# Optimization experiments

Hardware: AMD Instinct MI355X
Metric: run time of the kernel (lower is better)

The kernel has to match this reference:

```python
import jax, jax.numpy as jnp
import numpy as np

B, N, DIM, H, K = 2, 8192, 256, 8, 32
HD = DIM // H


def setup_inputs() -> dict:
    key = jax.random.key(0)
    ks = jax.random.split(key, 10)
    s = 1.0 / np.sqrt(DIM)
    return {
        "x": jax.random.normal(ks[0], (B, N, DIM), jnp.float32),
        "xyz": jax.random.normal(ks[1], (B, N, 3), jnp.float32),
        "idx": jax.random.randint(ks[2], (B, N, K), 0, N, jnp.int32),
        "Wq": jax.random.normal(ks[3], (DIM, DIM), jnp.float32) * s,
        "bq": jnp.zeros((DIM,), jnp.float32),
        "Wk": jax.random.normal(ks[4], (DIM, DIM), jnp.float32) * s,
        "bk": jnp.zeros((DIM,), jnp.float32),
        "Wv": jax.random.normal(ks[5], (DIM, DIM), jnp.float32) * s,
        "bv": jnp.zeros((DIM,), jnp.float32),
        "Wo": jax.random.normal(ks[6], (DIM, DIM), jnp.float32) * s,
        "bo": jnp.zeros((DIM,), jnp.float32),
        "W1": jax.random.normal(ks[7], (3, 32), jnp.float32) * 0.5,
        "b1": jnp.zeros((32,), jnp.float32),
        "W2": jax.random.normal(ks[8], (32, H), jnp.float32) * 0.2,
        "b2": jnp.zeros((H,), jnp.float32),
    }


def reference(x, xyz, idx, Wq, bq, Wk, bk, Wv, bv, Wo, bo, W1, b1, W2, b2):
    Bn, Nn, C = x.shape
    k = idx.shape[-1]
    q = (x @ Wq + bq).reshape(Bn, Nn, H, HD)          # [B,N,H,hd]
    kf = (x @ Wk + bk).reshape(Bn, Nn, H, HD)
    vf = (x @ Wv + bv).reshape(Bn, Nn, H, HD)
    # gather k neighbors per point (per-batch fancy indexing)
    gather = jax.vmap(lambda f, i: f[i])               # [N,H,hd],[N,k] -> [N,k,H,hd]
    kn = gather(kf, idx)                               # [B,N,k,H,hd]
    vn = gather(vf, idx)
    nxyz = jax.vmap(lambda p, i: p[i])(xyz, idx)       # [B,N,k,3]
    rel = xyz[:, :, None, :] - nxyz                    # [B,N,k,3]
    bias = jax.nn.relu(rel @ W1 + b1) @ W2 + b2        # [B,N,k,H]
    scores = jnp.einsum('bnhd,bnkhd->bnhk', q, kn) / np.sqrt(HD).astype(np.float32)
    scores = scores + bias.transpose(0, 1, 3, 2)       # [B,N,H,k]
    attn = jax.nn.softmax(scores, axis=-1)
    out = jnp.einsum('bnhk,bnkhd->bnhd', attn, vn).reshape(Bn, Nn, C)
    return out @ Wo + bo
```

## Files before the change

kernel.cpp:

```cpp
#include <hip/hip_runtime.h>
#include <hip/hip_bf16.h>

typedef unsigned int uint32;
typedef unsigned short ushort;
typedef __attribute__((ext_vector_type(4))) float floatx4;
typedef __attribute__((ext_vector_type(8))) __bf16 bf16x8;

#define NPTS 8192
#define HSZ 524288

__device__ __forceinline__ ushort f2bf(float f) {
    uint32 u = __float_as_uint(f);
    uint32 r = (u + 0x7fffu + ((u >> 16) & 1u)) >> 16;
    return (ushort)r;
}
__device__ __forceinline__ float bf1(ushort u) { return __uint_as_float((uint32)u << 16); }
__device__ __forceinline__ float bflo(uint32 u) { return __uint_as_float(u << 16); }
__device__ __forceinline__ float bfhi(uint32 u) { return __uint_as_float(u & 0xffff0000u); }

__global__ __launch_bounds__(256) void prep_kernel(
    const float* __restrict__ x, const float* __restrict__ xyz, const int* __restrict__ idx,
    const float* __restrict__ Wq, const float* __restrict__ Wk,
    const float* __restrict__ Wv, const float* __restrict__ Wo,
    const float* __restrict__ bq, const float* __restrict__ bk, const float* __restrict__ bv,
    const float* __restrict__ W1, const float* __restrict__ b1,
    const float* __restrict__ W2, const float* __restrict__ b2,
    ushort* __restrict__ xb, ushort* __restrict__ Wqkvt, ushort* __restrict__ Wot,
    float* __restrict__ biasqkv, ushort* __restrict__ bias_hg, uint32* __restrict__ offs) {
    const int bi = blockIdx.x;
    const int tid = threadIdx.x;
    if (bi < 4096) {
        int i = (bi * 256 + tid) * 4;
        float4 v = *(const float4*)(x + i);
        ushort4 o;
        o.x = f2bf(v.x); o.y = f2bf(v.y); o.z = f2bf(v.z); o.w = f2bf(v.w);
        *(ushort4*)(xb + i) = o;
    } else if (bi < 5120) {
        int f = (bi - 4096) * 256 + tid;
        if (f < 768 * 256) {
            int n = f >> 8, k = f & 255;
            int seg = n >> 8, nc = n & 255;
            const float* W = (seg == 0) ? Wq : (seg == 1) ? Wk : Wv;
            Wqkvt[f] = f2bf(W[k * 256 + nc]);
        } else {
            int g = f - 768 * 256;
            int n = g >> 8, k = g & 255;
            Wot[g] = f2bf(Wo[k * 256 + n]);
        }
        if (f < 768) biasqkv[f] = (f < 256) ? bq[f] : (f < 512) ? bk[f - 256] : bv[f - 512];
    } else {
        __shared__ float W1s[96], b1s[32], W2s[256], b2s[8];
        if (tid < 96) W1s[tid] = W1[tid];
        if (tid < 32) b1s[tid] = b1[tid];
        W2s[tid] = W2[tid];
        if (tid < 8) b2s[tid] = b2[tid];
        __syncthreads();
        const int wid = tid >> 6, lane = tid & 63;
        const int s = lane >> 5, j = lane & 31;
        const int p = (bi - 5120) * 8 + wid * 2 + s;
        const int b = p >> 13, n = p & 8191;
        const int nj = idx[(size_t)p * 32 + j];
        offs[(size_t)p * 32 + j] = (uint32)(nj + b * NPTS) * 64u;
        const size_t pb = ((size_t)b * NPTS + n) * 3;
        const size_t nb = ((size_t)b * NPTS + nj) * 3;
        const float rx = xyz[pb + 0] - xyz[nb + 0];
        const float ry = xyz[pb + 1] - xyz[nb + 1];
        const float rz = xyz[pb + 2] - xyz[nb + 2];
        float acc[8];
#pragma unroll
        for (int h = 0; h < 8; ++h) acc[h] = b2s[h];
#pragma unroll
        for (int u = 0; u < 32; ++u) {
            float hv = rx * W1s[u] + ry * W1s[32 + u] + rz * W1s[64 + u] + b1s[u];
            hv = fmaxf(hv, 0.f);
#pragma unroll
            for (int h = 0; h < 8; ++h) acc[h] += hv * W2s[u * 8 + h];
        }
#pragma unroll
        for (int h = 0; h < 8; ++h) bias_hg[(size_t)h * HSZ + p * 32 + j] = f2bf(acc[h]);
    }
}

__global__ __launch_bounds__(256) void gemm_qkv(const ushort* __restrict__ A,
                                                const ushort* __restrict__ Wt,
                                                const float* __restrict__ bias,
                                                ushort* __restrict__ qh, ushort* __restrict__ kh,
                                                ushort* __restrict__ vh) {
    __shared__ __align__(16) ushort As[128 * 64];
    __shared__ __align__(16) ushort Bs[128 * 64];
    const int tid = threadIdx.x;
    const int w = tid >> 6, lane = tid & 63;
    const int m0 = blockIdx.y * 128, n0 = blockIdx.x * 128;
    const int wm = (w & 1) * 64, wn = (w >> 1) * 64;

    floatx4 acc[4][4] = {};

    for (int kt = 0; kt < 256; kt += 64) {
        __syncthreads();
#pragma unroll
        for (int c4 = 0; c4 < 4; ++c4) {
            const int c = w * 4 + c4;
            const int r = c * 8 + (lane >> 3);
            const int gseg = (lane & 7) ^ (r & 7);
            const char* ga = (const char*)(A + (size_t)(m0 + r) * 256 + kt) + gseg * 16;
            const char* gb = (const char*)(Wt + (size_t)(n0 + r) * 256 + kt) + gseg * 16;
            __builtin_amdgcn_global_load_lds((const __attribute__((address_space(1))) void*)ga,
                                             (__attribute__((address_space(3))) void*)((char*)As + c * 1024),
                                             16, 0, 0);
            __builtin_amdgcn_global_load_lds((const __attribute__((address_space(1))) void*)gb,
                                             (__attribute__((address_space(3))) void*)((char*)Bs + c * 1024),
                                             16, 0, 0);
        }
        __syncthreads();

        bf16x8 af[2][4], bg[2][4];
#pragma unroll
        for (int kk = 0; kk < 2; ++kk) {
            const int s = kk * 4 + (lane >> 4);
            const int phys = s ^ (lane & 7);
#pragma unroll
            for (int i = 0; i < 4; ++i) {
                af[kk][i] = *(const bf16x8*)((const char*)As + (wm + i * 16 + (lane & 15)) * 128 + phys * 16);
                bg[kk][i] = *(const bf16x8*)((const char*)Bs + (wn + i * 16 + (lane & 15)) * 128 + phys * 16);
            }
        }
#pragma unroll
        for (int kk = 0; kk < 2; ++kk)
#pragma unroll
            for (int fi = 0; fi < 4; ++fi)
#pragma unroll
                for (int pi = 0; pi < 4; ++pi)
                    acc[fi][pi] = __builtin_amdgcn_mfma_f32_16x16x32_bf16(bg[kk][fi], af[kk][pi], acc[fi][pi], 0, 0, 0);
    }

#pragma unroll
    for (int fi = 0; fi < 4; ++fi) {
        const int gf0 = n0 + wn + fi * 16 + (lane >> 4) * 4;
        const int seg = gf0 >> 8;
        const int head = (gf0 >> 5) & 7;
        const int dim0 = gf0 & 31;
        ushort* segp = (seg == 0) ? qh : (seg == 1) ? kh : vh;
        const float b0 = bias[gf0 + 0], b1v = bias[gf0 + 1];
        const float b2v = bias[gf0 + 2], b3v = bias[gf0 + 3];
#pragma unroll
        for (int pi = 0; pi < 4; ++pi) {
            const int pt = m0 + wm + pi * 16 + (lane & 15);
            uint2 o;
            o.x = (uint32)f2bf(acc[fi][pi][0] + b0) | ((uint32)f2bf(acc[fi][pi][1] + b1v) << 16);
            o.y = (uint32)f2bf(acc[fi][pi][2] + b2v) | ((uint32)f2bf(acc[fi][pi][3] + b3v) << 16);
            *(uint2*)(segp + (size_t)head * HSZ + (size_t)pt * 32 + dim0) = o;
        }
    }
}

__global__ __launch_bounds__(256) void gemm_mfma64(const ushort* __restrict__ A,
                                                   const ushort* __restrict__ Wt,
                                                   const float* __restrict__ bias,
                                                   float* __restrict__ outv, int N) {
    __shared__ __align__(16) ushort As[64 * 32];
    __shared__ __align__(16) ushort Bs[64 * 32];
    const int tid = threadIdx.x;
    const int w = tid >> 6, lane = tid & 63;
    const int m0 = blockIdx.y * 64, n0 = blockIdx.x * 64;
    const int row = tid >> 2;
    const int col16 = (tid & 3) * 16;

    floatx4 acc[4] = {};

    for (int kt = 0; kt < 256; kt += 32) {
        __syncthreads();
        {
            const char* ga = (const char*)(A + (size_t)(m0 + row) * 256 + kt) + col16;
            const char* gb = (const char*)(Wt + (size_t)(n0 + row) * 256 + kt) + col16;
            __builtin_amdgcn_global_load_lds((const __attribute__((address_space(1))) void*)ga,
                                             (__attribute__((address_space(3))) void*)((char*)As + w * 1024),
                                             16, 0, 0);
            __builtin_amdgcn_global_load_lds((const __attribute__((address_space(1))) void*)gb,
                                             (__attribute__((address_space(3))) void*)((char*)Bs + w * 1024),
                                             16, 0, 0);
        }
        __syncthreads();

        bf16x8 af = *(const bf16x8*)&As[(w * 16 + (lane & 15)) * 32 + (lane >> 4) * 8];
        bf16x8 bg[4];
#pragma unroll
        for (int ni = 0; ni < 4; ++ni)
            bg[ni] = *(const bf16x8*)&Bs[(ni * 16 + (lane & 15)) * 32 + (lane >> 4) * 8];
#pragma unroll
        for (int ni = 0; ni < 4; ++ni)
            acc[ni] = __builtin_amdgcn_mfma_f32_16x16x32_bf16(af, bg[ni], acc[ni], 0, 0, 0);
    }

#pragma unroll
    for (int ni = 0; ni < 4; ++ni) {
        const int col = n0 + ni * 16 + (lane & 15);
        const float bv = bias[col];
        const int row0 = m0 + w * 16 + (lane >> 4) * 4;
#pragma unroll
        for (int r = 0; r < 4; ++r)
            outv[(size_t)(row0 + r) * N + col] = acc[ni][r] + bv;
    }
}

__global__ __launch_bounds__(256) void attn_kernel(
    const ushort* __restrict__ qh, const ushort* __restrict__ kh, const ushort* __restrict__ vh,
    const uint32* __restrict__ offs, const ushort* __restrict__ bias_hg, ushort* __restrict__ out) {
    __shared__ __align__(16) float q_s[4][2][32];
    __shared__ float e_s[4][2][32];
    __shared__ uint32 off_s[4][2][32];
    __shared__ float ssum_s[4][2];

    const int tid = threadIdx.x, wid = tid >> 6, lane = tid & 63;
    const int h = blockIdx.x >> 11;
    const int pg = blockIdx.x & 2047;
    const int pbase = pg * 8 + wid * 2;

    const char* kh_h = (const char*)(kh + (size_t)h * HSZ);
    const char* vh_h = (const char*)(vh + (size_t)h * HSZ);

    const int s = lane >> 5, j = lane & 31;
    const int p = pbase + s;

    const uint32 off = offs[(size_t)p * 32 + j];
    off_s[wid][s][j] = off;
    q_s[wid][s][j] = bf1(qh[(size_t)h * HSZ + p * 32 + j]);
    __syncthreads();

    {
        const uint4* kp = (const uint4*)(kh_h + off);
        float d = 0.f;
#pragma unroll
        for (int c = 0; c < 4; ++c) {
            uint4 kv = kp[c];
            float4 qa = *(const float4*)&q_s[wid][s][c * 8];
            float4 qb = *(const float4*)&q_s[wid][s][c * 8 + 4];
            d += bflo(kv.x) * qa.x + bfhi(kv.x) * qa.y
               + bflo(kv.y) * qa.z + bfhi(kv.y) * qa.w
               + bflo(kv.z) * qb.x + bfhi(kv.z) * qb.y
               + bflo(kv.w) * qb.z + bfhi(kv.w) * qb.w;
        }
        const float sc = d * 0.17677669529663687f + bf1(bias_hg[(size_t)h * HSZ + p * 32 + j]);
        const float e = __expf(sc);
        float ssum = e;
#pragma unroll
        for (int msk = 16; msk >= 1; msk >>= 1) ssum += __shfl_xor(ssum, msk, 64);
        e_s[wid][s][j] = e;
        if (j == 0) ssum_s[wid][s] = ssum;
    }
    __syncthreads();

    {
        const int s2 = lane >> 5, hj = (lane >> 4) & 1, d2 = lane & 15;
        const int p2 = pbase + s2;
        const float rinv = __builtin_amdgcn_rcpf(ssum_s[wid][s2]);
        float ax = 0.f, ay = 0.f;
#pragma unroll
        for (int jj = 0; jj < 16; ++jj) {
            const int j2 = hj * 16 + jj;
            const float wgt = e_s[wid][s2][j2];
            const uint32 v = *(const uint32*)(vh_h + off_s[wid][s2][j2] + d2 * 4);
            ax += wgt * bflo(v);
            ay += wgt * bfhi(v);
        }
        ax += __shfl_xor(ax, 16, 64);
        ay += __shfl_xor(ay, 16, 64);
        if (hj == 0) {
            const uint32 o = (uint32)f2bf(ax * rinv) | ((uint32)f2bf(ay * rinv) << 16);
            *(uint32*)(out + (size_t)p2 * 256 + h * 32 + d2 * 2) = o;
        }
    }
}

extern "C" void kernel_launch(void* const* d_in, const int* in_sizes, int n_in,
                              void* d_out, int out_size, void* d_ws, size_t ws_size,
                              hipStream_t stream) {
    const float* x   = (const float*)d_in[0];
    const float* xyz = (const float*)d_in[1];
    const int*   idx = (const int*)d_in[2];
    const float* Wq = (const float*)d_in[3];
    const float* bq = (const float*)d_in[4];
    const float* Wk = (const float*)d_in[5];
    const float* bk = (const float*)d_in[6];
    const float* Wv = (const float*)d_in[7];
    const float* bv = (const float*)d_in[8];
    const float* Wo = (const float*)d_in[9];
    const float* bo = (const float*)d_in[10];
    const float* W1 = (const float*)d_in[11];
    const float* b1 = (const float*)d_in[12];
    const float* W2 = (const float*)d_in[13];
    const float* b2 = (const float*)d_in[14];

    char* wsb = (char*)d_ws;
    ushort* x_bf    = (ushort*)wsb;
    ushort* aout_bf = x_bf;
    ushort* qh      = (ushort*)(wsb + 8388608);
    ushort* kh      = (ushort*)(wsb + 16777216);
    ushort* vh      = (ushort*)(wsb + 25165824);
    ushort* bias_hg = (ushort*)(wsb + 33554432);
    ushort* Wqkvt   = (ushort*)(wsb + 41943040);
    ushort* Wot     = (ushort*)(wsb + 42336256);
    float*  biasqkv = (float*)(wsb + 42467328);
    uint32* offs    = (uint32*)(wsb + 42471424);

    prep_kernel<<<7168, 256, 0, stream>>>(x, xyz, idx, Wq, Wk, Wv, Wo, bq, bk, bv,
                                          W1, b1, W2, b2, x_bf, Wqkvt, Wot, biasqkv,
                                          bias_hg, offs);

    gemm_qkv<<<dim3(6, 128), 256, 0, stream>>>(x_bf, Wqkvt, biasqkv, qh, kh, vh);

    attn_kernel<<<16384, 256, 0, stream>>>(qh, kh, vh, offs, bias_hg, aout_bf);

    gemm_mfma64<<<dim3(4, 256), 256, 0, stream>>>(aout_bf, Wot, bo, (float*)d_out, 256);
}
```

Baseline: 184.5 us.

## Remap attention kernel to one lane per point with register-held query

The attention kernel now runs one 64-thread wave per block. Each block covers 32 points of one head, and each lane owns one point and half of its neighbours (for scores) or half of the head dimension (for the weighted V sum). The query and bias are loaded into registers with wide vector loads. Neighbour offsets are staged in padded LDS, and the V accumulation uses 16-byte loads instead of 4-byte ones. This removes the block-wide barriers and cross-lane shuffle reductions and cuts instruction overhead, at the cost of many more registers per lane and lower per-instruction coalescing of the gathered rows.

```diff
diff --git a/kernel.cpp b/kernel.cpp
--- a/kernel.cpp
+++ b/kernel.cpp
@@ -202,72 +202,108 @@
     }
 }
 
-__global__ __launch_bounds__(256) void attn_kernel(
+__global__ __launch_bounds__(64, 4) void attn_kernel(
     const ushort* __restrict__ qh, const ushort* __restrict__ kh, const ushort* __restrict__ vh,
     const uint32* __restrict__ offs, const ushort* __restrict__ bias_hg, ushort* __restrict__ out) {
-    __shared__ __align__(16) float q_s[4][2][32];
-    __shared__ float e_s[4][2][32];
-    __shared__ uint32 off_s[4][2][32];
-    __shared__ float ssum_s[4][2];
-
-    const int tid = threadIdx.x, wid = tid >> 6, lane = tid & 63;
-    const int h = blockIdx.x >> 11;
-    const int pg = blockIdx.x & 2047;
-    const int pbase = pg * 8 + wid * 2;
+    __shared__ uint32 off_s[32][33];
+    __shared__ float e_s[32][33];
+
+    const int lane = threadIdx.x;
+    const int h = blockIdx.x >> 9;
+    const int pg = blockIdx.x & 511;
+    const int pbase = pg * 32;
 
     const char* kh_h = (const char*)(kh + (size_t)h * HSZ);
     const char* vh_h = (const char*)(vh + (size_t)h * HSZ);
 
-    const int s = lane >> 5, j = lane & 31;
-    const int p = pbase + s;
-
-    const uint32 off = offs[(size_t)p * 32 + j];
-    off_s[wid][s][j] = off;
-    q_s[wid][s][j] = bf1(qh[(size_t)h * HSZ + p * 32 + j]);
-    __syncthreads();
-
     {
+        const int sp = lane >> 1, sj = (lane & 1) * 16;
+        const uint4* gsrc = (const uint4*)(offs + ((size_t)(pbase + sp) * 32 + sj));
+#pragma unroll
+        for (int c = 0; c < 4; ++c) {
+            uint4 v = gsrc[c];
+            off_s[sj + c * 4 + 0][sp] = v.x;
+            off_s[sj + c * 4 + 1][sp] = v.y;
+            off_s[sj + c * 4 + 2][sp] = v.z;
+            off_s[sj + c * 4 + 3][sp] = v.w;
+        }
+    }
+
+    const int p = lane & 31, jh = lane >> 5;
+
+    float qq[32];
+    {
+        const uint4* qp = (const uint4*)(qh + (size_t)h * HSZ + (size_t)(pbase + p) * 32);
+#pragma unroll
+        for (int c = 0; c < 4; ++c) {
+            uint4 v = qp[c];
+            qq[c * 8 + 0] = bflo(v.x); qq[c * 8 + 1] = bfhi(v.x);
+            qq[c * 8 + 2] = bflo(v.y); qq[c * 8 + 3] = bfhi(v.y);
+            qq[c * 8 + 4] = bflo(v.z); qq[c * 8 + 5] = bfhi(v.z);
+            qq[c * 8 + 6] = bflo(v.w); qq[c * 8 + 7] = bfhi(v.w);
+        }
+    }
+    uint32 bb[8];
+    {
+        const uint4* bp = (const uint4*)(bias_hg + (size_t)h * HSZ + (size_t)(pbase + p) * 32 + jh * 16);
+        uint4 v0 = bp[0], v1 = bp[1];
+        bb[0] = v0.x; bb[1] = v0.y; bb[2] = v0.z; bb[3] = v0.w;
+        bb[4] = v1.x; bb[5] = v1.y; bb[6] = v1.z; bb[7] = v1.w;
+    }
+
+    float psum = 0.f;
+#pragma unroll
+    for (int t = 0; t < 16; ++t) {
+        const int j = jh * 16 + t;
+        const uint32 off = off_s[j][p];
         const uint4* kp = (const uint4*)(kh_h + off);
         float d = 0.f;
 #pragma unroll
         for (int c = 0; c < 4; ++c) {
             uint4 kv = kp[c];
-            float4 qa = *(const float4*)&q_s[wid][s][c * 8];
-            float4 qb = *(const float4*)&q_s[wid][s][c * 8 + 4];
-            d += bflo(kv.x) * qa.x + bfhi(kv.x) * qa.y
-               + bflo(kv.y) * qa.z + bfhi(kv.y) * qa.w
-               + bflo(kv.z) * qb.x + bfhi(kv.z) * qb.y
-               + bflo(kv.w) * qb.z + bfhi(kv.w) * qb.w;
-        }
-        const float sc = d * 0.17677669529663687f + bf1(bias_hg[(size_t)h * HSZ + p * 32 + j]);
-        const float e = __expf(sc);
-        float ssum = e;
-#pragma unroll
-        for (int msk = 16; msk >= 1; msk >>= 1) ssum += __shfl_xor(ssum, msk, 64);
-        e_s[wid][s][j] = e;
-        if (j == 0) ssum_s[wid][s] = ssum;
-    }
-    __syncthreads();
-
+            d += bflo(kv.x) * qq[c * 8 + 0] + bfhi(kv.x) * qq[c * 8 + 1]
+               + bflo(kv.y) * qq[c * 8 + 2] + bfhi(kv.y) * qq[c * 8 + 3]
+               + bflo(kv.z) * qq[c * 8 + 4] + bfhi(kv.z) * qq[c * 8 + 5]
+               + bflo(kv.w) * qq[c * 8 + 6] + bfhi(kv.w) * qq[c * 8 + 7];
+        }
+        const float bval = (t & 1) ? bfhi(bb[t >> 1]) : bflo(bb[t >> 1]);
+        const float e = __expf(d * 0.17677669529663687f + bval);
+        e_s[j][p] = e;
+        psum += e;
+    }
+    psum += __shfl_xor(psum, 32, 64);
+    const float rinv = __builtin_amdgcn_rcpf(psum);
+
+    const int dh = jh;
+    float a[16] = {};
+#pragma unroll
+    for (int j = 0; j < 32; ++j) {
+        const uint32 off = off_s[j][p];
+        const float wgt = e_s[j][p];
+        const uint4* vp = (const uint4*)(vh_h + off + dh * 32);
+        uint4 v0 = vp[0], v1 = vp[1];
+        a[0] += wgt * bflo(v0.x); a[1] += wgt * bfhi(v0.x);
+        a[2] += wgt * bflo(v0.y); a[3] += wgt * bfhi(v0.y);
+        a[4] += wgt * bflo(v0.z); a[5] += wgt * bfhi(v0.z);
+        a[6] += wgt * bflo(v0.w); a[7] += wgt * bfhi(v0.w);
+        a[8] += wgt * bflo(v1.x); a[9] += wgt * bfhi(v1.x);
+        a[10] += wgt * bflo(v1.y); a[11] += wgt * bfhi(v1.y);
+        a[12] += wgt * bflo(v1.z); a[13] += wgt * bfhi(v1.z);
+        a[14] += wgt * bflo(v1.w); a[15] += wgt * bfhi(v1.w);
+    }
     {
-        const int s2 = lane >> 5, hj = (lane >> 4) & 1, d2 = lane & 15;
-        const int p2 = pbase + s2;
-        const float rinv = __builtin_amdgcn_rcpf(ssum_s[wid][s2]);
-        float ax = 0.f, ay = 0.f;
-#pragma unroll
-        for (int jj = 0; jj < 16; ++jj) {
-            const int j2 = hj * 16 + jj;
-            const float wgt = e_s[wid][s2][j2];
-            const uint32 v = *(const uint32*)(vh_h + off_s[wid][s2][j2] + d2 * 4);
-            ax += wgt * bflo(v);
-            ay += wgt * bfhi(v);
-        }
-        ax += __shfl_xor(ax, 16, 64);
-        ay += __shfl_xor(ay, 16, 64);
-        if (hj == 0) {
-            const uint32 o = (uint32)f2bf(ax * rinv) | ((uint32)f2bf(ay * rinv) << 16);
-            *(uint32*)(out + (size_t)p2 * 256 + h * 32 + d2 * 2) = o;
-        }
+        uint4 o0, o1;
+        o0.x = (uint32)f2bf(a[0] * rinv) | ((uint32)f2bf(a[1] * rinv) << 16);
+        o0.y = (uint32)f2bf(a[2] * rinv) | ((uint32)f2bf(a[3] * rinv) << 16);
+        o0.z = (uint32)f2bf(a[4] * rinv) | ((uint32)f2bf(a[5] * rinv) << 16);
+        o0.w = (uint32)f2bf(a[6] * rinv) | ((uint32)f2bf(a[7] * rinv) << 16);
+        o1.x = (uint32)f2bf(a[8] * rinv) | ((uint32)f2bf(a[9] * rinv) << 16);
+        o1.y = (uint32)f2bf(a[10] * rinv) | ((uint32)f2bf(a[11] * rinv) << 16);
+        o1.z = (uint32)f2bf(a[12] * rinv) | ((uint32)f2bf(a[13] * rinv) << 16);
+        o1.w = (uint32)f2bf(a[14] * rinv) | ((uint32)f2bf(a[15] * rinv) << 16);
+        uint4* op = (uint4*)(out + (size_t)(pbase + p) * 256 + h * 32 + dh * 16);
+        op[0] = o0;
+        op[1] = o1;
     }
 }
 
@@ -308,7 +344,7 @@
 
     gemm_qkv<<<dim3(6, 128), 256, 0, stream>>>(x_bf, Wqkvt, biasqkv, qh, kh, vh);
 
-    attn_kernel<<<16384, 256, 0, stream>>>(qh, kh, vh, offs, bias_hg, aout_bf);
+    attn_kernel<<<4096, 64, 0, stream>>>(qh, kh, vh, offs, bias_hg, aout_bf);
 
     gemm_mfma64<<<dim3(4, 256), 256, 0, stream>>>(aout_bf, Wot, bo, (float*)d_out, 256);
 }
```

Measured after the change: 367.8 us. +99.3%, slower.

## Split attention kernel into separate score/softmax and weighted-V gather kernels

Applied to the files above, without the earlier changes.

Splits the fused attention kernel into two launches. The first computes scores and softmax weights and writes the normalized weights in bf16, overwriting the positional bias buffer. The second reads offsets and weights straight into registers and gathers V. This removes the intermediate LDS traffic and the second block barrier, and lets each kernel use fewer registers. In exchange it adds a launch and an extra round trip of the weights through global memory, and normalizing in bf16 before the V sum changes rounding slightly.

```diff
diff --git a/kernel.cpp b/kernel.cpp
--- a/kernel.cpp
+++ b/kernel.cpp
@@ -202,13 +202,10 @@
     }
 }
 
-__global__ __launch_bounds__(256) void attn_kernel(
-    const ushort* __restrict__ qh, const ushort* __restrict__ kh, const ushort* __restrict__ vh,
-    const uint32* __restrict__ offs, const ushort* __restrict__ bias_hg, ushort* __restrict__ out) {
+__global__ __launch_bounds__(256) void attn_score(
+    const ushort* __restrict__ qh, const ushort* __restrict__ kh,
+    const uint32* __restrict__ offs, ushort* __restrict__ wgt) {
     __shared__ __align__(16) float q_s[4][2][32];
-    __shared__ float e_s[4][2][32];
-    __shared__ uint32 off_s[4][2][32];
-    __shared__ float ssum_s[4][2];
 
     const int tid = threadIdx.x, wid = tid >> 6, lane = tid & 63;
     const int h = blockIdx.x >> 11;
@@ -216,58 +213,78 @@
     const int pbase = pg * 8 + wid * 2;
 
     const char* kh_h = (const char*)(kh + (size_t)h * HSZ);
-    const char* vh_h = (const char*)(vh + (size_t)h * HSZ);
 
     const int s = lane >> 5, j = lane & 31;
     const int p = pbase + s;
 
     const uint32 off = offs[(size_t)p * 32 + j];
-    off_s[wid][s][j] = off;
     q_s[wid][s][j] = bf1(qh[(size_t)h * HSZ + p * 32 + j]);
+    const float bias = bf1(wgt[(size_t)h * HSZ + p * 32 + j]);
     __syncthreads();
 
+    const uint4* kp = (const uint4*)(kh_h + off);
+    float d = 0.f;
+#pragma unroll
+    for (int c = 0; c < 4; ++c) {
+        uint4 kv = kp[c];
+        float4 qa = *(const float4*)&q_s[wid][s][c * 8];
+        float4 qb = *(const float4*)&q_s[wid][s][c * 8 + 4];
+        d += bflo(kv.x) * qa.x + bfhi(kv.x) * qa.y
+           + bflo(kv.y) * qa.z + bfhi(kv.y) * qa.w
+           + bflo(kv.z) * qb.x + bfhi(kv.z) * qb.y
+           + bflo(kv.w) * qb.z + bfhi(kv.w) * qb.w;
+    }
+    const float sc = d * 0.17677669529663687f + bias;
+    const float e = __expf(sc);
+    float ssum = e;
+#pragma unroll
+    for (int msk = 16; msk >= 1; msk >>= 1) ssum += __shfl_xor(ssum, msk, 64);
+    const float rinv = __builtin_amdgcn_rcpf(ssum);
+    wgt[(size_t)h * HSZ + p * 32 + j] = f2bf(e * rinv);
+}
+
+__global__ __launch_bounds__(256) void attn_pv(
+    const ushort* __restrict__ vh, const uint32* __restrict__ offs,
+    const ushort* __restrict__ wgt, ushort* __restrict__ out) {
+    const int tid = threadIdx.x, wid = tid >> 6, lane = tid & 63;
+    const int h = blockIdx.x >> 11;
+    const int pg = blockIdx.x & 2047;
+    const int p = pg * 8 + wid * 2 + (lane >> 5);
+    const int hj = (lane >> 4) & 1, d2 = lane & 15;
+
+    const char* vh_h = (const char*)(vh + (size_t)h * HSZ);
+
+    uint32 oa[16];
     {
-        const uint4* kp = (const uint4*)(kh_h + off);
-        float d = 0.f;
+        const uint4* op = (const uint4*)(offs + (size_t)p * 32 + hj * 16);
 #pragma unroll
         for (int c = 0; c < 4; ++c) {
-            uint4 kv = kp[c];
-            float4 qa = *(const float4*)&q_s[wid][s][c * 8];
-            float4 qb = *(const float4*)&q_s[wid][s][c * 8 + 4];
-            d += bflo(kv.x) * qa.x + bfhi(kv.x) * qa.y
-               + bflo(kv.y) * qa.z + bfhi(kv.y) * qa.w
-               + bflo(kv.z) * qb.x + bfhi(kv.z) * qb.y
-               + bflo(kv.w) * qb.z + bfhi(kv.w) * qb.w;
-        }
-        const float sc = d * 0.17677669529663687f + bf1(bias_hg[(size_t)h * HSZ + p * 32 + j]);
-        const float e = __expf(sc);
-        float ssum = e;
-#pragma unroll
-        for (int msk = 16; msk >= 1; msk >>= 1) ssum += __shfl_xor(ssum, msk, 64);
-        e_s[wid][s][j] = e;
-        if (j == 0) ssum_s[wid][s] = ssum;
-    }
-    __syncthreads();
-
+            uint4 v = op[c];
+            oa[c * 4 + 0] = v.x; oa[c * 4 + 1] = v.y;
+            oa[c * 4 + 2] = v.z; oa[c * 4 + 3] = v.w;
+        }
+    }
+    float wa[16];
     {
-        const int s2 = lane >> 5, hj = (lane >> 4) & 1, d2 = lane & 15;
-        const int p2 = pbase + s2;
-        const float rinv = __builtin_amdgcn_rcpf(ssum_s[wid][s2]);
-        float ax = 0.f, ay = 0.f;
-#pragma unroll
-        for (int jj = 0; jj < 16; ++jj) {
-            const int j2 = hj * 16 + jj;
-            const float wgt = e_s[wid][s2][j2];
-            const uint32 v = *(const uint32*)(vh_h + off_s[wid][s2][j2] + d2 * 4);
-            ax += wgt * bflo(v);
-            ay += wgt * bfhi(v);
-        }
-        ax += __shfl_xor(ax, 16, 64);
-        ay += __shfl_xor(ay, 16, 64);
-        if (hj == 0) {
-            const uint32 o = (uint32)f2bf(ax * rinv) | ((uint32)f2bf(ay * rinv) << 16);
-            *(uint32*)(out + (size_t)p2 * 256 + h * 32 + d2 * 2) = o;
-        }
+        const uint4* wp = (const uint4*)(wgt + (size_t)h * HSZ + p * 32 + hj * 16);
+        uint4 w0 = wp[0], w1 = wp[1];
+        uint32 ww[8] = {w0.x, w0.y, w0.z, w0.w, w1.x, w1.y, w1.z, w1.w};
+#pragma unroll
+        for (int i = 0; i < 8; ++i) { wa[2 * i] = bflo(ww[i]); wa[2 * i + 1] = bfhi(ww[i]); }
+    }
+
+    float ax = 0.f, ay = 0.f;
+#pragma unroll
+    for (int jj = 0; jj < 16; ++jj) {
+        const uint32 v = *(const uint32*)(vh_h + oa[jj] + d2 * 4);
+        ax += wa[jj] * bflo(v);
+        ay += wa[jj] * bfhi(v);
+    }
+    ax += __shfl_xor(ax, 16, 64);
+    ay += __shfl_xor(ay, 16, 64);
+    if (hj == 0) {
+        const uint32 o = (uint32)f2bf(ax) | ((uint32)f2bf(ay) << 16);
+        *(uint32*)(out + (size_t)p * 256 + h * 32 + d2 * 2) = o;
     }
 }
 
@@ -308,7 +325,9 @@
 
     gemm_qkv<<<dim3(6, 128), 256, 0, stream>>>(x_bf, Wqkvt, biasqkv, qh, kh, vh);
 
-    attn_kernel<<<16384, 256, 0, stream>>>(qh, kh, vh, offs, bias_hg, aout_bf);
+    attn_score<<<16384, 256, 0, stream>>>(qh, kh, offs, bias_hg);
+
+    attn_pv<<<16384, 256, 0, stream>>>(vh, offs, bias_hg, aout_bf);
 
     gemm_mfma64<<<dim3(4, 256), 256, 0, stream>>>(aout_bf, Wot, bo, (float*)d_out, 256);
 }
```

New measurement: 190.6 us. +3.3%, slower.
